# Kernel tuning notes

Hardware: AMD Instinct MI355X
Metric: run time of the kernel (lower is better)

The kernel has to match this reference:

```python
import jax, jax.numpy as jnp
import numpy as np

N = 100000
E = 1600000
D_IN = 128
F = 128


def _glorot(key, shape, scale=1.0):
    fan_in, fan_out = shape
    std = jnp.sqrt(2.0 / (fan_in + fan_out))
    return jax.random.normal(key, shape, dtype=jnp.float32) * std * scale


def setup_inputs() -> dict:
    key = jax.random.key(0)
    ks = jax.random.split(key, 10)
    h = jax.random.normal(ks[0], (N, D_IN), dtype=jnp.float32)
    # ensure every node appears as a row (src) so degree >= 1 (no inf in deg**-0.5)
    src_extra = jax.random.randint(ks[1], (E - N,), 0, N, dtype=jnp.int32)
    edge_src = jnp.concatenate([jnp.arange(N, dtype=jnp.int32), src_extra])
    edge_dst = jax.random.randint(ks[2], (E,), 0, N, dtype=jnp.int32)
    # faithful to original: fake indices sampled in [0, E) (jnp indexing clamps)
    src_fake = jax.random.randint(ks[3], (E,), 0, E, dtype=jnp.int32)
    dst_fake = jax.random.randint(ks[4], (E,), 0, E, dtype=jnp.int32)
    w_gcn0 = _glorot(ks[5], (D_IN, F))
    w_gcn1 = _glorot(ks[6], (F, F))
    # small scale on rate0 head to keep exp(sum over F dims) finite in fp32
    w_rate0 = _glorot(ks[7], (F, F), scale=0.05)
    w_rate1 = _glorot(ks[8], (F, 1))
    w_alpha = _glorot(ks[9], (F, 1))
    return {"h": h, "w_gcn0": w_gcn0, "w_gcn1": w_gcn1, "w_rate0": w_rate0,
            "w_rate1": w_rate1, "w_alpha": w_alpha, "edge_src": edge_src,
            "edge_dst": edge_dst, "src_fake": src_fake, "dst_fake": dst_fake}


def _gcn(h, W, norm, edge_src, edge_dst):
    h = h * norm                     # [N, d] degree pre-norm
    h = h @ W                        # dense projection
    h = jax.ops.segment_sum(h[edge_dst], edge_src, num_segments=N)  # a @ h
    return h * norm                  # degree post-norm


def reference(h, w_gcn0, w_gcn1, w_rate0, w_rate1, w_alpha,
              edge_src, edge_dst, src_fake, dst_fake):
    ones = jnp.ones((E,), dtype=h.dtype)
    deg = jax.ops.segment_sum(ones, edge_src, num_segments=N)  # row sums of a
    norm = (deg ** -0.5)[:, None]

    h = _gcn(h, w_gcn0, norm, edge_src, edge_dst)
    h = _gcn(h, w_gcn1, norm, edge_src, edge_dst)

    rate0 = h @ w_rate0   # [N, F]
    rate1 = h @ w_rate1   # [N, 1]
    alpha = h @ w_alpha   # [N, 1]

    src, dst = edge_src, edge_dst
    rate0_real = jnp.exp((rate0[src] + rate0[dst]).sum(-1))
    rate1_real = jnp.exp((rate1[src] + rate1[dst]).sum(-1))
    alpha_real = jax.nn.sigmoid((alpha[src] * alpha[dst]).sum(-1) / alpha.shape[-1] ** 0.5)

    # faithful to original (including rate0+rate1 mix and /shape (not sqrt) in alpha_fake)
    rate0_fake = jnp.exp((rate0[src_fake] + rate1[dst_fake]).sum(-1))
    rate1_fake = jnp.exp((rate1[src_fake] + rate1[dst_fake]).sum(-1))
    alpha_fake = jax.nn.sigmoid((alpha[src] * alpha[dst_fake]).sum(-1) / alpha.shape[-1])

    return jnp.stack([rate0_real, rate1_real, alpha_real,
                      rate0_fake, rate1_fake, alpha_fake])  # [6, E]
```

## Files before the change

kernel.cpp:

```cpp
#include <hip/hip_runtime.h>
#include <hip/hip_bf16.h>
#include <math.h>

#define NN 100000
#define EE 1600000
#define KB 256
#define RR 391
#define CAP 8192


__global__ __launch_bounds__(256) void k_initcur(int* __restrict__ gcur) {
    gcur[threadIdx.x] = threadIdx.x * CAP;
}


__global__ __launch_bounds__(256) void k_partA(const int* __restrict__ src, const int* __restrict__ dst,
                                               int* __restrict__ gcur, unsigned int* __restrict__ pk, int E) {
    __shared__ int cnt[KB];
    __shared__ int base[KB];
    int t = threadIdx.x;
    int e0 = blockIdx.x * 4096;
    cnt[t] = 0;
    __syncthreads();
    unsigned int pkv[16];
    int bkt[16];
    #pragma unroll
    for (int i = 0; i < 16; ++i) {
        int e = e0 + i * 256 + t;
        if (e < E) {
            int s = src[e];
            int d = dst[e];
            int b = s / RR;
            bkt[i] = b;
            pkv[i] = (unsigned int)d | ((unsigned int)(s - b * RR) << 17);
            atomicAdd(&cnt[b], 1);
        } else {
            bkt[i] = -1;
        }
    }
    __syncthreads();
    base[t] = (cnt[t] > 0) ? atomicAdd(&gcur[t], cnt[t]) : 0;
    __syncthreads();
    cnt[t] = 0;
    __syncthreads();
    #pragma unroll
    for (int i = 0; i < 16; ++i) {
        if (bkt[i] >= 0) {
            int r = atomicAdd(&cnt[bkt[i]], 1);
            int pos = base[bkt[i]] + r;
            if (pos < (bkt[i] + 1) * CAP) pk[pos] = pkv[i];
        }
    }
}


__global__ __launch_bounds__(128) void k_pmat(const float* __restrict__ w_gcn0,
                                              const float* __restrict__ w_gcn1,
                                              const float* __restrict__ w_rate0,
                                              const float* __restrict__ w_rate1,
                                              const float* __restrict__ w_alpha,
                                              float* __restrict__ Pt0, float* __restrict__ Pt1,
                                              float* __restrict__ Pt2) {
    __shared__ float V0[128], V1[128], V2[128];
    __shared__ float Q0[128], Q1[128], Q2[128];
    int t = threadIdx.x;
    float s = 0.f;
    for (int j = 0; j < 128; ++j) s += w_rate0[t * 128 + j];
    V0[t] = s;
    V1[t] = w_rate1[t];
    V2[t] = w_alpha[t];
    __syncthreads();
    {
        float q0 = 0.f, q1 = 0.f, q2 = 0.f;
        for (int k = 0; k < 128; ++k) {
            float w = w_gcn1[t * 128 + k];
            q0 += w * V0[k];
            q1 += w * V1[k];
            q2 += w * V2[k];
        }
        Q0[t] = q0; Q1[t] = q1; Q2[t] = q2;
    }
    __syncthreads();
    {
        float p0 = 0.f, p1 = 0.f, p2 = 0.f;
        for (int m = 0; m < 128; ++m) {
            float w = w_gcn0[t * 128 + m];
            p0 += w * Q0[m];
            p1 += w * Q1[m];
            p2 += w * Q2[m];
        }
        Pt0[t] = p0; Pt1[t] = p1; Pt2[t] = p2;
    }
}


__global__ __launch_bounds__(1024) void k_cnt_proj(const unsigned int* __restrict__ pk,
                                                   const int* __restrict__ gcur,
                                                   const float* __restrict__ h,
                                                   const float* __restrict__ Pt0, const float* __restrict__ Pt1,
                                                   const float* __restrict__ Pt2,
                                                   float* __restrict__ nrm, float4* __restrict__ w4, int n) {
    __shared__ int c[RR];
    __shared__ float s_nrm[RR];
    __shared__ float sP0[128], sP1[128], sP2[128];
    int b = blockIdx.x;
    int t = threadIdx.x;
    int nlo = b * RR;
    int nhi = nlo + RR; if (nhi > n) nhi = n;
    if (nlo >= n) return;
    int nn = nhi - nlo;
    if (t < 128) { sP0[t] = Pt0[t]; sP1[t] = Pt1[t]; sP2[t] = Pt2[t]; }
    for (int i = t; i < RR; i += 1024) c[i] = 0;
    __syncthreads();
    int P0 = b * CAP;
    int m = gcur[b] - P0;
    for (int i = t; i < m; i += 1024) atomicAdd(&c[pk[P0 + i] >> 17], 1);
    __syncthreads();
    for (int i = t; i < nn; i += 1024) {
        float nv = rsqrtf((float)c[i]);
        s_nrm[i] = nv;
        nrm[nlo + i] = nv;
    }
    __syncthreads();
    int hw = t >> 5;
    int l32 = t & 31;
    int c4 = l32 * 4;
    float4 c0 = *(const float4*)(sP0 + c4);
    float4 c1 = *(const float4*)(sP1 + c4);
    float4 c2 = *(const float4*)(sP2 + c4);
    for (int i0 = 0; i0 < nn; i0 += 32) {
        int i = i0 + hw;
        if (i >= nn) break;
        int node = nlo + i;
        float4 hv = *(const float4*)(h + (size_t)node * 128 + c4);
        float p0 = hv.x * c0.x + hv.y * c0.y + hv.z * c0.z + hv.w * c0.w;
        float p1 = hv.x * c1.x + hv.y * c1.y + hv.z * c1.z + hv.w * c1.w;
        float p2 = hv.x * c2.x + hv.y * c2.y + hv.z * c2.z + hv.w * c2.w;
        #pragma unroll
        for (int off = 16; off > 0; off >>= 1) {
            p0 += __shfl_down(p0, off, 32);
            p1 += __shfl_down(p1, off, 32);
            p2 += __shfl_down(p2, off, 32);
        }
        if (l32 == 0) {
            float nv = s_nrm[i];
            w4[node] = make_float4(nv * p0, nv * p1, nv * p2, 0.f);
        }
    }
}


__global__ __launch_bounds__(1024) void k_agg(const unsigned int* __restrict__ pk,
                                              const int* __restrict__ gcur,
                                              const float4* __restrict__ T, const float* __restrict__ nrm,
                                              float4* __restrict__ outv, int n, int mode) {
    __shared__ float s0[RR], s1[RR], s2[RR];
    int b = blockIdx.x;
    int t = threadIdx.x;
    int nlo = b * RR;
    int nhi = nlo + RR; if (nhi > n) nhi = n;
    if (nlo >= n) return;
    for (int i = t; i < RR; i += 1024) { s0[i] = 0.f; s1[i] = 0.f; s2[i] = 0.f; }
    __syncthreads();
    int P0 = b * CAP;
    int m = gcur[b] - P0;
    for (int i = t; i < m; i += 1024) {
        unsigned int w = pk[P0 + i];
        int srel = (int)(w >> 17);
        float4 v = T[w & 0x1FFFFu];
        atomicAdd(&s0[srel], v.x);
        atomicAdd(&s1[srel], v.y);
        atomicAdd(&s2[srel], v.z);
    }
    __syncthreads();
    int nn = nhi - nlo;
    for (int i = t; i < nn; i += 1024) {
        int node = nlo + i;
        float nv = nrm[node];
        float sc = (mode == 1) ? nv * nv : nv;
        outv[node] = make_float4(sc * s0[i], sc * s1[i], sc * s2[i], 0.f);
    }
}


__global__ __launch_bounds__(256) void k_edge_out(const int* __restrict__ esrc, const int* __restrict__ edst,
                                                  const int* __restrict__ sfake, const int* __restrict__ dfake,
                                                  const float4* __restrict__ p4, float* __restrict__ out,
                                                  int E, int n) {
    int e = blockIdx.x * 256 + threadIdx.x;
    if (e >= E) return;
    int s = esrc[e], d = edst[e];
    int sf = sfake[e]; sf = sf < 0 ? 0 : (sf >= n ? n - 1 : sf);
    int df = dfake[e]; df = df < 0 ? 0 : (df >= n ? n - 1 : df);
    float4 ps = p4[s], pd = p4[d], psf = p4[sf], pdf = p4[df];
    out[e]                 = expf(ps.x + pd.x);
    out[(size_t)E + e]     = expf(ps.y + pd.y);
    out[(size_t)2 * E + e] = 1.f / (1.f + expf(-(ps.z * pd.z)));
    out[(size_t)3 * E + e] = expf(psf.x + 128.f * pdf.y);
    out[(size_t)4 * E + e] = expf(psf.y + pdf.y);
    out[(size_t)5 * E + e] = 1.f / (1.f + expf(-(ps.z * pdf.z)));
}


extern "C" void kernel_launch(void* const* d_in, const int* in_sizes, int n_in,
                              void* d_out, int out_size, void* d_ws, size_t ws_size,
                              hipStream_t stream) {
    const float* h       = (const float*)d_in[0];
    const float* w_gcn0  = (const float*)d_in[1];
    const float* w_gcn1  = (const float*)d_in[2];
    const float* w_rate0 = (const float*)d_in[3];
    const float* w_rate1 = (const float*)d_in[4];
    const float* w_alpha = (const float*)d_in[5];
    const int* edge_src  = (const int*)d_in[6];
    const int* edge_dst  = (const int*)d_in[7];
    const int* src_fake  = (const int*)d_in[8];
    const int* dst_fake  = (const int*)d_in[9];
    float* out = (float*)d_out;

    const int N = NN, E = EE;

    char* p = (char*)d_ws;
    auto alloc = [&](size_t bytes) {
        char* r = p;
        p += (bytes + 255) & ~(size_t)255;
        return r;
    };
    unsigned int* pk = (unsigned int*)alloc((size_t)KB * CAP * 4);
    int* gcur   = (int*)alloc(KB * 4);
    float* nrm  = (float*)alloc((size_t)N * 4);
    float4* w4  = (float4*)alloc((size_t)N * 16);
    float4* z4  = (float4*)alloc((size_t)N * 16);
    float4* p4  = (float4*)alloc((size_t)N * 16);
    float* Pt0  = (float*)alloc(512);
    float* Pt1  = (float*)alloc(512);
    float* Pt2  = (float*)alloc(512);

    int ebl4k = (E + 4095) / 4096;
    int ebl = (E + 255) / 256;

    k_initcur<<<1, KB, 0, stream>>>(gcur);
    k_partA<<<ebl4k, 256, 0, stream>>>(edge_src, edge_dst, gcur, pk, E);
    k_pmat<<<1, 128, 0, stream>>>(w_gcn0, w_gcn1, w_rate0, w_rate1, w_alpha, Pt0, Pt1, Pt2);
    k_cnt_proj<<<KB, 1024, 0, stream>>>(pk, gcur, h, Pt0, Pt1, Pt2, nrm, w4, N);
    k_agg<<<KB, 1024, 0, stream>>>(pk, gcur, w4, nrm, z4, N, 1);
    k_agg<<<KB, 1024, 0, stream>>>(pk, gcur, z4, nrm, p4, N, 2);
    k_edge_out<<<ebl, 256, 0, stream>>>(edge_src, edge_dst, src_fake, dst_fake, p4, out, E, N);
}
```

Measured before the change: 238.6 us.

## Restructure pipeline: global degree atomics, split aggregation blocks, parallel weight fold

Node degrees are now counted with global atomics while partitioning edges, so the projection kernel can run over 782 small blocks instead of 256 bucket blocks. Each aggregation bucket is split across two 512-thread blocks that merge into the output with global atomics, and the norm is stored in the .w lane so scaling is applied on the consumer side. The weight-folding kernel uses 1024 threads with shuffle reductions, and a memset replaces the cursor-init kernel. The trade is many more global atomics, both on deg during partitioning and on the output vectors, plus a float summation order that is no longer deterministic.

Measured after the change: 296.2 us. 24.2% more time.

```diff
diff --git a/kernel.cpp b/kernel.cpp
--- a/kernel.cpp
+++ b/kernel.cpp
@@ -1,5 +1,4 @@
 #include <hip/hip_runtime.h>
-#include <hip/hip_bf16.h>
 #include <math.h>
 
 #define NN 100000
@@ -9,13 +8,60 @@
 #define CAP 8192
 
 
-__global__ __launch_bounds__(256) void k_initcur(int* __restrict__ gcur) {
-    gcur[threadIdx.x] = threadIdx.x * CAP;
-}
-
-
-__global__ __launch_bounds__(256) void k_partA(const int* __restrict__ src, const int* __restrict__ dst,
-                                               int* __restrict__ gcur, unsigned int* __restrict__ pk, int E) {
+__global__ __launch_bounds__(1024) void k_pmat(const float* __restrict__ w_gcn0,
+                                               const float* __restrict__ w_gcn1,
+                                               const float* __restrict__ w_rate0,
+                                               const float* __restrict__ w_rate1,
+                                               const float* __restrict__ w_alpha,
+                                               float* __restrict__ Pt0, float* __restrict__ Pt1,
+                                               float* __restrict__ Pt2) {
+    __shared__ float V0[128], V1[128], V2[128];
+    __shared__ float Q0[128], Q1[128], Q2[128];
+    int t = threadIdx.x;
+    int r = t >> 3, seg = t & 7;
+    {
+        const float* p = w_rate0 + r * 128 + seg * 16;
+        float s = 0.f;
+        #pragma unroll
+        for (int k = 0; k < 16; ++k) s += p[k];
+        s += __shfl_down(s, 4, 8); s += __shfl_down(s, 2, 8); s += __shfl_down(s, 1, 8);
+        if (seg == 0) V0[r] = s;
+    }
+    if (t < 128) { V1[t] = w_rate1[t]; V2[t] = w_alpha[t]; }
+    __syncthreads();
+    {
+        const float* p = w_gcn1 + r * 128 + seg * 16;
+        float q0 = 0.f, q1 = 0.f, q2 = 0.f;
+        #pragma unroll
+        for (int k = 0; k < 16; ++k) {
+            float w = p[k]; int j = seg * 16 + k;
+            q0 += w * V0[j]; q1 += w * V1[j]; q2 += w * V2[j];
+        }
+        q0 += __shfl_down(q0, 4, 8); q0 += __shfl_down(q0, 2, 8); q0 += __shfl_down(q0, 1, 8);
+        q1 += __shfl_down(q1, 4, 8); q1 += __shfl_down(q1, 2, 8); q1 += __shfl_down(q1, 1, 8);
+        q2 += __shfl_down(q2, 4, 8); q2 += __shfl_down(q2, 2, 8); q2 += __shfl_down(q2, 1, 8);
+        if (seg == 0) { Q0[r] = q0; Q1[r] = q1; Q2[r] = q2; }
+    }
+    __syncthreads();
+    {
+        const float* p = w_gcn0 + r * 128 + seg * 16;
+        float q0 = 0.f, q1 = 0.f, q2 = 0.f;
+        #pragma unroll
+        for (int k = 0; k < 16; ++k) {
+            float w = p[k]; int j = seg * 16 + k;
+            q0 += w * Q0[j]; q1 += w * Q1[j]; q2 += w * Q2[j];
+        }
+        q0 += __shfl_down(q0, 4, 8); q0 += __shfl_down(q0, 2, 8); q0 += __shfl_down(q0, 1, 8);
+        q1 += __shfl_down(q1, 4, 8); q1 += __shfl_down(q1, 2, 8); q1 += __shfl_down(q1, 1, 8);
+        q2 += __shfl_down(q2, 4, 8); q2 += __shfl_down(q2, 2, 8); q2 += __shfl_down(q2, 1, 8);
+        if (seg == 0) { Pt0[r] = q0; Pt1[r] = q1; Pt2[r] = q2; }
+    }
+}
+
+
+__global__ __launch_bounds__(256) void k_part(const int* __restrict__ src, const int* __restrict__ dst,
+                                              int* __restrict__ gcur, int* __restrict__ deg,
+                                              unsigned int* __restrict__ pk, int E) {
     __shared__ int cnt[KB];
     __shared__ int base[KB];
     int t = threadIdx.x;
@@ -34,92 +80,42 @@
             bkt[i] = b;
             pkv[i] = (unsigned int)d | ((unsigned int)(s - b * RR) << 17);
             atomicAdd(&cnt[b], 1);
-        } else {
-            bkt[i] = -1;
-        }
-    }
-    __syncthreads();
-    base[t] = (cnt[t] > 0) ? atomicAdd(&gcur[t], cnt[t]) : 0;
+            atomicAdd(&deg[s], 1);
+        } else bkt[i] = -1;
+    }
+    __syncthreads();
+    base[t] = cnt[t] ? atomicAdd(&gcur[t], cnt[t]) : 0;
     __syncthreads();
     cnt[t] = 0;
     __syncthreads();
     #pragma unroll
     for (int i = 0; i < 16; ++i) {
         if (bkt[i] >= 0) {
-            int r = atomicAdd(&cnt[bkt[i]], 1);
-            int pos = base[bkt[i]] + r;
-            if (pos < (bkt[i] + 1) * CAP) pk[pos] = pkv[i];
-        }
-    }
-}
-
-
-__global__ __launch_bounds__(128) void k_pmat(const float* __restrict__ w_gcn0,
-                                              const float* __restrict__ w_gcn1,
-                                              const float* __restrict__ w_rate0,
-                                              const float* __restrict__ w_rate1,
-                                              const float* __restrict__ w_alpha,
-                                              float* __restrict__ Pt0, float* __restrict__ Pt1,
-                                              float* __restrict__ Pt2) {
-    __shared__ float V0[128], V1[128], V2[128];
-    __shared__ float Q0[128], Q1[128], Q2[128];
-    int t = threadIdx.x;
-    float s = 0.f;
-    for (int j = 0; j < 128; ++j) s += w_rate0[t * 128 + j];
-    V0[t] = s;
-    V1[t] = w_rate1[t];
-    V2[t] = w_alpha[t];
-    __syncthreads();
-    {
-        float q0 = 0.f, q1 = 0.f, q2 = 0.f;
-        for (int k = 0; k < 128; ++k) {
-            float w = w_gcn1[t * 128 + k];
-            q0 += w * V0[k];
-            q1 += w * V1[k];
-            q2 += w * V2[k];
-        }
-        Q0[t] = q0; Q1[t] = q1; Q2[t] = q2;
-    }
-    __syncthreads();
-    {
-        float p0 = 0.f, p1 = 0.f, p2 = 0.f;
-        for (int m = 0; m < 128; ++m) {
-            float w = w_gcn0[t * 128 + m];
-            p0 += w * Q0[m];
-            p1 += w * Q1[m];
-            p2 += w * Q2[m];
-        }
-        Pt0[t] = p0; Pt1[t] = p1; Pt2[t] = p2;
-    }
-}
-
-
-__global__ __launch_bounds__(1024) void k_cnt_proj(const unsigned int* __restrict__ pk,
-                                                   const int* __restrict__ gcur,
-                                                   const float* __restrict__ h,
-                                                   const float* __restrict__ Pt0, const float* __restrict__ Pt1,
-                                                   const float* __restrict__ Pt2,
-                                                   float* __restrict__ nrm, float4* __restrict__ w4, int n) {
-    __shared__ int c[RR];
-    __shared__ float s_nrm[RR];
-    __shared__ float sP0[128], sP1[128], sP2[128];
-    int b = blockIdx.x;
-    int t = threadIdx.x;
-    int nlo = b * RR;
-    int nhi = nlo + RR; if (nhi > n) nhi = n;
-    if (nlo >= n) return;
-    int nn = nhi - nlo;
-    if (t < 128) { sP0[t] = Pt0[t]; sP1[t] = Pt1[t]; sP2[t] = Pt2[t]; }
-    for (int i = t; i < RR; i += 1024) c[i] = 0;
-    __syncthreads();
-    int P0 = b * CAP;
-    int m = gcur[b] - P0;
-    for (int i = t; i < m; i += 1024) atomicAdd(&c[pk[P0 + i] >> 17], 1);
-    __syncthreads();
-    for (int i = t; i < nn; i += 1024) {
-        float nv = rsqrtf((float)c[i]);
-        s_nrm[i] = nv;
-        nrm[nlo + i] = nv;
+            int rr = atomicAdd(&cnt[bkt[i]], 1);
+            int rel = base[bkt[i]] + rr;
+            if (rel < CAP) pk[bkt[i] * CAP + rel] = pkv[i];
+        }
+    }
+}
+
+
+__global__ __launch_bounds__(256) void k_proj(const int* __restrict__ deg, const float* __restrict__ h,
+                                              const float* __restrict__ Pt0, const float* __restrict__ Pt1,
+                                              const float* __restrict__ Pt2,
+                                              float4* __restrict__ w4, float4* __restrict__ z4,
+                                              float4* __restrict__ p4) {
+    __shared__ float sP0[128], sP1[128], sP2[128], snrm[128];
+    int t = threadIdx.x;
+    int nlo = blockIdx.x * 128;
+    if (t < 128) {
+        sP0[t] = Pt0[t]; sP1[t] = Pt1[t]; sP2[t] = Pt2[t];
+        int node = nlo + t;
+        if (node < NN) {
+            float nv = rsqrtf((float)deg[node]);
+            snrm[t] = nv;
+            z4[node] = make_float4(0.f, 0.f, 0.f, nv * nv);
+            p4[node] = make_float4(0.f, 0.f, 0.f, nv);
+        }
     }
     __syncthreads();
     int hw = t >> 5;
@@ -128,77 +124,93 @@
     float4 c0 = *(const float4*)(sP0 + c4);
     float4 c1 = *(const float4*)(sP1 + c4);
     float4 c2 = *(const float4*)(sP2 + c4);
-    for (int i0 = 0; i0 < nn; i0 += 32) {
+    #pragma unroll 4
+    for (int i0 = 0; i0 < 128; i0 += 8) {
         int i = i0 + hw;
-        if (i >= nn) break;
         int node = nlo + i;
-        float4 hv = *(const float4*)(h + (size_t)node * 128 + c4);
-        float p0 = hv.x * c0.x + hv.y * c0.y + hv.z * c0.z + hv.w * c0.w;
-        float p1 = hv.x * c1.x + hv.y * c1.y + hv.z * c1.z + hv.w * c1.w;
-        float p2 = hv.x * c2.x + hv.y * c2.y + hv.z * c2.z + hv.w * c2.w;
-        #pragma unroll
-        for (int off = 16; off > 0; off >>= 1) {
-            p0 += __shfl_down(p0, off, 32);
-            p1 += __shfl_down(p1, off, 32);
-            p2 += __shfl_down(p2, off, 32);
-        }
-        if (l32 == 0) {
-            float nv = s_nrm[i];
-            w4[node] = make_float4(nv * p0, nv * p1, nv * p2, 0.f);
-        }
-    }
-}
-
-
-__global__ __launch_bounds__(1024) void k_agg(const unsigned int* __restrict__ pk,
-                                              const int* __restrict__ gcur,
-                                              const float4* __restrict__ T, const float* __restrict__ nrm,
-                                              float4* __restrict__ outv, int n, int mode) {
+        if (node < NN) {
+            float4 hv = *(const float4*)(h + (size_t)node * 128 + c4);
+            float p0v = hv.x * c0.x + hv.y * c0.y + hv.z * c0.z + hv.w * c0.w;
+            float p1v = hv.x * c1.x + hv.y * c1.y + hv.z * c1.z + hv.w * c1.w;
+            float p2v = hv.x * c2.x + hv.y * c2.y + hv.z * c2.z + hv.w * c2.w;
+            #pragma unroll
+            for (int off = 16; off > 0; off >>= 1) {
+                p0v += __shfl_down(p0v, off, 32);
+                p1v += __shfl_down(p1v, off, 32);
+                p2v += __shfl_down(p2v, off, 32);
+            }
+            if (l32 == 0) {
+                float nv = snrm[i];
+                w4[node] = make_float4(nv * p0v, nv * p1v, nv * p2v, 0.f);
+            }
+        }
+    }
+}
+
+
+template<int MODE>
+__global__ __launch_bounds__(512) void k_agg(const unsigned int* __restrict__ pk,
+                                             const int* __restrict__ gcur,
+                                             const float4* __restrict__ T,
+                                             float4* __restrict__ outv) {
     __shared__ float s0[RR], s1[RR], s2[RR];
-    int b = blockIdx.x;
-    int t = threadIdx.x;
+    int b = blockIdx.x >> 1;
+    int half = blockIdx.x & 1;
+    int t = threadIdx.x;
+    if (t < RR) { s0[t] = 0.f; s1[t] = 0.f; s2[t] = 0.f; }
+    __syncthreads();
+    int m = gcur[b]; if (m > CAP) m = CAP;
+    int mh = m >> 1;
+    int lo = half ? mh : 0;
+    int hi = half ? m : mh;
+    const unsigned int* P = pk + b * CAP;
+    for (int i = lo + t; i < hi; i += 512) {
+        unsigned int w = P[i];
+        float4 v = T[w & 0x1FFFFu];
+        float x = v.x, y = v.y, z = v.z;
+        if (MODE == 2) { x *= v.w; y *= v.w; z *= v.w; }
+        int srel = (int)(w >> 17);
+        atomicAdd(&s0[srel], x);
+        atomicAdd(&s1[srel], y);
+        atomicAdd(&s2[srel], z);
+    }
+    __syncthreads();
     int nlo = b * RR;
-    int nhi = nlo + RR; if (nhi > n) nhi = n;
-    if (nlo >= n) return;
-    for (int i = t; i < RR; i += 1024) { s0[i] = 0.f; s1[i] = 0.f; s2[i] = 0.f; }
-    __syncthreads();
-    int P0 = b * CAP;
-    int m = gcur[b] - P0;
-    for (int i = t; i < m; i += 1024) {
-        unsigned int w = pk[P0 + i];
-        int srel = (int)(w >> 17);
-        float4 v = T[w & 0x1FFFFu];
-        atomicAdd(&s0[srel], v.x);
-        atomicAdd(&s1[srel], v.y);
-        atomicAdd(&s2[srel], v.z);
-    }
-    __syncthreads();
-    int nn = nhi - nlo;
-    for (int i = t; i < nn; i += 1024) {
-        int node = nlo + i;
-        float nv = nrm[node];
-        float sc = (mode == 1) ? nv * nv : nv;
-        outv[node] = make_float4(sc * s0[i], sc * s1[i], sc * s2[i], 0.f);
-    }
-}
-
-
-__global__ __launch_bounds__(256) void k_edge_out(const int* __restrict__ esrc, const int* __restrict__ edst,
-                                                  const int* __restrict__ sfake, const int* __restrict__ dfake,
-                                                  const float4* __restrict__ p4, float* __restrict__ out,
-                                                  int E, int n) {
-    int e = blockIdx.x * 256 + threadIdx.x;
-    if (e >= E) return;
-    int s = esrc[e], d = edst[e];
-    int sf = sfake[e]; sf = sf < 0 ? 0 : (sf >= n ? n - 1 : sf);
-    int df = dfake[e]; df = df < 0 ? 0 : (df >= n ? n - 1 : df);
-    float4 ps = p4[s], pd = p4[d], psf = p4[sf], pdf = p4[df];
-    out[e]                 = expf(ps.x + pd.x);
-    out[(size_t)E + e]     = expf(ps.y + pd.y);
-    out[(size_t)2 * E + e] = 1.f / (1.f + expf(-(ps.z * pd.z)));
-    out[(size_t)3 * E + e] = expf(psf.x + 128.f * pdf.y);
-    out[(size_t)4 * E + e] = expf(psf.y + pdf.y);
-    out[(size_t)5 * E + e] = 1.f / (1.f + expf(-(ps.z * pdf.z)));
+    int nn = NN - nlo; if (nn > RR) nn = RR;
+    for (int i = t; i < nn; i += 512) {
+        float* o = (float*)&outv[nlo + i];
+        atomicAdd(o + 0, s0[i]);
+        atomicAdd(o + 1, s1[i]);
+        atomicAdd(o + 2, s2[i]);
+    }
+}
+
+
+__global__ __launch_bounds__(256) void k_edge(const int* __restrict__ esrc, const int* __restrict__ edst,
+                                              const int* __restrict__ sfake, const int* __restrict__ dfake,
+                                              const float4* __restrict__ p4, float* __restrict__ out, int E) {
+    int t = threadIdx.x;
+    int e00 = blockIdx.x * 512 + t;
+    #pragma unroll
+    for (int k = 0; k < 2; ++k) {
+        int e = e00 + k * 256;
+        if (e < E) {
+            int s = esrc[e], d = edst[e];
+            int sf = sfake[e]; sf = sf < 0 ? 0 : (sf >= NN ? NN - 1 : sf);
+            int df = dfake[e]; df = df < 0 ? 0 : (df >= NN ? NN - 1 : df);
+            float4 ps = p4[s], pd = p4[d], psf = p4[sf], pdf = p4[df];
+            float psx = ps.w * ps.x, psy = ps.w * ps.y, psz = ps.w * ps.z;
+            float pdx = pd.w * pd.x, pdy = pd.w * pd.y, pdz = pd.w * pd.z;
+            float sfx = psf.w * psf.x, sfy = psf.w * psf.y;
+            float dfy = pdf.w * pdf.y, dfz = pdf.w * pdf.z;
+            out[e]                  = expf(psx + pdx);
+            out[(size_t)EE + e]     = expf(psy + pdy);
+            out[(size_t)2 * EE + e] = 1.f / (1.f + expf(-(psz * pdz)));
+            out[(size_t)3 * EE + e] = expf(sfx + 128.f * dfy);
+            out[(size_t)4 * EE + e] = expf(sfy + dfy);
+            out[(size_t)5 * EE + e] = 1.f / (1.f + expf(-(psz * dfz)));
+        }
+    }
 }
 
 
@@ -217,7 +229,7 @@
     const int* dst_fake  = (const int*)d_in[9];
     float* out = (float*)d_out;
 
-    const int N = NN, E = EE;
+    const int E = EE;
 
     char* p = (char*)d_ws;
     auto alloc = [&](size_t bytes) {
@@ -226,23 +238,22 @@
         return r;
     };
     unsigned int* pk = (unsigned int*)alloc((size_t)KB * CAP * 4);
-    int* gcur   = (int*)alloc(KB * 4);
-    float* nrm  = (float*)alloc((size_t)N * 4);
-    float4* w4  = (float4*)alloc((size_t)N * 16);
-    float4* z4  = (float4*)alloc((size_t)N * 16);
-    float4* p4  = (float4*)alloc((size_t)N * 16);
+    int* ctrl   = (int*)alloc((size_t)(KB + NN) * 4);
+    int* gcur   = ctrl;
+    int* deg    = ctrl + KB;
+    float4* w4  = (float4*)alloc((size_t)NN * 16);
+    float4* z4  = (float4*)alloc((size_t)NN * 16);
+    float4* p4  = (float4*)alloc((size_t)NN * 16);
     float* Pt0  = (float*)alloc(512);
     float* Pt1  = (float*)alloc(512);
     float* Pt2  = (float*)alloc(512);
 
-    int ebl4k = (E + 4095) / 4096;
-    int ebl = (E + 255) / 256;
-
-    k_initcur<<<1, KB, 0, stream>>>(gcur);
-    k_partA<<<ebl4k, 256, 0, stream>>>(edge_src, edge_dst, gcur, pk, E);
-    k_pmat<<<1, 128, 0, stream>>>(w_gcn0, w_gcn1, w_rate0, w_rate1, w_alpha, Pt0, Pt1, Pt2);
-    k_cnt_proj<<<KB, 1024, 0, stream>>>(pk, gcur, h, Pt0, Pt1, Pt2, nrm, w4, N);
-    k_agg<<<KB, 1024, 0, stream>>>(pk, gcur, w4, nrm, z4, N, 1);
-    k_agg<<<KB, 1024, 0, stream>>>(pk, gcur, z4, nrm, p4, N, 2);
-    k_edge_out<<<ebl, 256, 0, stream>>>(edge_src, edge_dst, src_fake, dst_fake, p4, out, E, N);
-}
+    hipMemsetAsync(ctrl, 0, (size_t)(KB + NN) * 4, stream);
+
+    k_pmat<<<1, 1024, 0, stream>>>(w_gcn0, w_gcn1, w_rate0, w_rate1, w_alpha, Pt0, Pt1, Pt2);
+    k_part<<<(E + 4095) / 4096, 256, 0, stream>>>(edge_src, edge_dst, gcur, deg, pk, E);
+    k_proj<<<(NN + 127) / 128, 256, 0, stream>>>(deg, h, Pt0, Pt1, Pt2, w4, z4, p4);
+    k_agg<1><<<2 * KB, 512, 0, stream>>>(pk, gcur, w4, z4);
+    k_agg<2><<<2 * KB, 512, 0, stream>>>(pk, gcur, z4, p4);
+    k_edge<<<(E + 511) / 512, 256, 0, stream>>>(edge_src, edge_dst, src_fake, dst_fake, p4, out, E);
+}
```
